# Kernel optimization log

Hardware: AMD Instinct MI355X
Metric: run time of the kernel (lower is better)

Reference implementation:

```python
import jax, jax.numpy as jnp
import numpy as np

D_MODEL = 1024
NUM_HEADS = 16
D_K = D_MODEL // NUM_HEADS


def setup_inputs() -> dict:
    key = jax.random.key(0)
    ks = jax.random.split(key, 5)
    s = 1.0 / np.sqrt(D_MODEL)
    return {
        "x": jax.random.normal(ks[0], (2, 2048, D_MODEL), dtype=jnp.float32),
        "Wq": jax.random.normal(ks[1], (D_MODEL, D_MODEL), dtype=jnp.float32) * s,
        "bq": jnp.zeros((D_MODEL,), jnp.float32),
        "Wk": jax.random.normal(ks[2], (D_MODEL, D_MODEL), dtype=jnp.float32) * s,
        "bk": jnp.zeros((D_MODEL,), jnp.float32),
        "Wv": jax.random.normal(ks[3], (D_MODEL, D_MODEL), dtype=jnp.float32) * s,
        "bv": jnp.zeros((D_MODEL,), jnp.float32),
        "Wo": jax.random.normal(ks[4], (D_MODEL, D_MODEL), dtype=jnp.float32) * s,
        "bo": jnp.zeros((D_MODEL,), jnp.float32),
    }


def _rotate_half(t):
    t1, t2 = t[..., : D_K // 2], t[..., D_K // 2 :]
    return jnp.concatenate((-t2, t1), axis=-1)


def reference(x, Wq, bq, Wk, bk, Wv, bv, Wo, bo):
    B, S, D = x.shape
    H, dk = NUM_HEADS, D_K
    # RoPE tables: inv_freq over even dims, emb = cat(freqs, freqs)
    inv_freq = 1.0 / (10000.0 ** (jnp.arange(0, dk, 2, dtype=jnp.float32) / dk))
    pos = jnp.arange(S, dtype=jnp.float32)
    freqs = pos[:, None] * inv_freq[None, :]            # [S, dk/2]
    emb = jnp.concatenate((freqs, freqs), axis=-1)      # [S, dk]
    cos = jnp.cos(emb)[None, :, None, :]                # [1, S, 1, dk]
    sin = jnp.sin(emb)[None, :, None, :]

    q = (x @ Wq + bq).reshape(B, S, H, dk)
    k = (x @ Wk + bk).reshape(B, S, H, dk)
    v = (x @ Wv + bv).reshape(B, S, H, dk)

    q = q * cos + _rotate_half(q) * sin
    k = k * cos + _rotate_half(k) * sin

    # [B,H,S,S] scores, stable softmax, then weighted sum of V
    scores = jnp.einsum("bqhd,bkhd->bhqk", q, k) / jnp.sqrt(jnp.float32(dk))
    attn = jax.nn.softmax(scores, axis=-1)
    out = jnp.einsum("bhqk,bkhd->bqhd", attn, v).reshape(B, S, D)
    return out @ Wo + bo
```

## Files before the change

### kernel.cpp

```cpp
#include <hip/hip_runtime.h>
#include <hip/hip_bf16.h>
#include <math.h>

typedef __bf16 bf16_t;
typedef bf16_t bf16x4 __attribute__((ext_vector_type(4)));
typedef bf16_t bf16x8 __attribute__((ext_vector_type(8)));
typedef float f32x4 __attribute__((ext_vector_type(4)));

#define SEQ 2048
#define BATCH 2
#define NHEAD 16
#define DK 64
#define DMODEL 1024

#define GLOAD16(gsrc, ldst)                                                        \
    __builtin_amdgcn_global_load_lds(                                              \
        (const __attribute__((address_space(1))) void*)(gsrc),                     \
        (__attribute__((address_space(3))) void*)(ldst), 16, 0, 0)

__device__ __forceinline__ float exp2_hw(float x) {
#if __has_builtin(__builtin_amdgcn_exp2f)
    return __builtin_amdgcn_exp2f(x);
#else
    float r; asm("v_exp_f32 %0, %1" : "=v"(r) : "v"(x)); return r;
#endif
}

__global__ __launch_bounds__(256)
void prep_kernel(const float* __restrict__ x, bf16_t* __restrict__ y,
                 const float* __restrict__ W0, const float* __restrict__ W1,
                 const float* __restrict__ W2, const float* __restrict__ W3,
                 bf16_t* __restrict__ Wt, float2* __restrict__ cs) {
    __shared__ float t[32][33];
    const int id = blockIdx.x, tid = threadIdx.x;
    if (id < 4096) {
        int i = (id * 256 + tid) * 4;
        float4 v = *reinterpret_cast<const float4*>(x + i);
        bf16x4 o = { (bf16_t)v.x, (bf16_t)v.y, (bf16_t)v.z, (bf16_t)v.w };
        *reinterpret_cast<bf16x4*>(y + i) = o;
    } else if (id < 8192) {
        const int id2 = id - 4096;
        const int z = id2 >> 10, rem = id2 & 1023;
        const int n0 = (rem & 31) * 32, k0 = ((rem >> 5) & 31) * 32;
        const int tx = tid & 31, ty = tid >> 5;
        const float* W = (z == 0) ? W0 : (z == 1) ? W1 : (z == 2) ? W2 : W3;
        bf16_t* out = Wt + ((size_t)z << 20);
#pragma unroll
        for (int i = 0; i < 32; i += 8)
            t[ty + i][tx] = W[(size_t)(k0 + ty + i) * DMODEL + n0 + tx];
        __syncthreads();
#pragma unroll
        for (int i = 0; i < 32; i += 8)
            out[(size_t)(n0 + ty + i) * DMODEL + k0 + tx] = (bf16_t)t[tx][ty + i];
    } else {
        int idx = (id - 8192) * 256 + tid;
        int j = idx & 31, s = idx >> 5;
        float inv = powf(10000.0f, -(float)j / 32.0f);
        float ang = (float)s * inv;
        cs[idx] = make_float2(cosf(ang), sinf(ang));
    }
}

template<int NF>
__device__ __forceinline__ void gemm_core(const bf16_t* __restrict__ A,
                                          const bf16_t* __restrict__ Bt,
                                          int m0, int n0,
                                          bf16_t* As, bf16_t* Bs,
                                          f32x4 (&acc)[4][NF]) {
    const int tid = threadIdx.x, lane = tid & 63, wid = tid >> 6;
    const int wr = wid >> 1, wc = wid & 1;
    const int lm = lane & 15, lq = lane >> 4;
    constexpr int BROWS = NF * 32;
    constexpr int NT = DMODEL / 32;

    const int r_in = lane >> 2;
    const int csw  = (((lane & 3) ^ ((lane >> 3) & 3)) << 3);
    const bf16_t* Ag = A  + (size_t)(m0 + 32 * wid + r_in) * DMODEL + csw;
    const bf16_t* Bg = Bt + (size_t)(n0 + (NF * 8) * wid + r_in) * DMODEL + csw;
    const int cswr = ((lq ^ ((lm >> 1) & 3)) << 4);

    auto stage = [&](int t, int buf) {
        const int k0 = t * 32;
        bf16_t* a = As + buf * (128 * 32) + 32 * wid * 32;
        bf16_t* b = Bs + buf * (BROWS * 32) + (NF * 8) * wid * 32;
        GLOAD16(Ag + k0,               a);
        GLOAD16(Ag + 16 * DMODEL + k0, a + 16 * 32);
        GLOAD16(Bg + k0,               b);
        if constexpr (NF == 4) GLOAD16(Bg + 16 * DMODEL + k0, b + 16 * 32);
    };

    stage(0, 0);
    stage(1, 1);
    int cb = 0;
    for (int t = 0; t < NT; ++t) {
        if (t + 2 < NT) {
            int sb = cb + 2; if (sb >= 3) sb -= 3;
            stage(t + 2, sb);
            if constexpr (NF == 4) asm volatile("s_waitcnt vmcnt(8)" ::: "memory");
            else                   asm volatile("s_waitcnt vmcnt(6)" ::: "memory");
        } else if (t + 1 < NT) {
            if constexpr (NF == 4) asm volatile("s_waitcnt vmcnt(4)" ::: "memory");
            else                   asm volatile("s_waitcnt vmcnt(3)" ::: "memory");
        } else {
            asm volatile("s_waitcnt vmcnt(0)" ::: "memory");
        }
        __builtin_amdgcn_s_barrier();

        const char* pAs = (const char*)(As + cb * (128 * 32));
        const char* pBs = (const char*)(Bs + cb * (BROWS * 32));
        bf16x8 af[4], bfr[NF];
#pragma unroll
        for (int mf = 0; mf < 4; ++mf)
            af[mf] = *reinterpret_cast<const bf16x8*>(pAs + (wr * 64 + mf * 16 + lm) * 64 + cswr);
#pragma unroll
        for (int nf = 0; nf < NF; ++nf)
            bfr[nf] = *reinterpret_cast<const bf16x8*>(pBs + (wc * (NF * 16) + nf * 16 + lm) * 64 + cswr);
#pragma unroll
        for (int mf = 0; mf < 4; ++mf)
#pragma unroll
            for (int nf = 0; nf < NF; ++nf)
                acc[mf][nf] = __builtin_amdgcn_mfma_f32_16x16x32_bf16(af[mf], bfr[nf], acc[mf][nf], 0, 0, 0);

        asm volatile("" ::: "memory");
        __builtin_amdgcn_s_barrier();
        if (++cb == 3) cb = 0;
    }
}

__global__ __launch_bounds__(256)
void gemm_qkv_kernel(const bf16_t* __restrict__ xb, const bf16_t* __restrict__ wtqk,
                     const bf16_t* __restrict__ wtv,
                     const float* __restrict__ bq, const float* __restrict__ bk,
                     const float* __restrict__ bv,
                     bf16_t* __restrict__ qb, bf16_t* __restrict__ kb,
                     bf16_t* __restrict__ vtb, const float2* __restrict__ cs) {
    __shared__ bf16_t As[3 * 128 * 32];
    __shared__ bf16_t Bs[3 * 128 * 32];
    const int tid = threadIdx.x, lane = tid & 63, wid = tid >> 6;
    const int wr = wid >> 1, wc = wid & 1;
    const int lm = lane & 15, lq = lane >> 4;
    const int orig = blockIdx.x;
    const int id = (orig & 7) * 96 + (orig >> 3);
    f32x4 acc[4][4] = {};

    if (id < 512) {
        const int m0 = (id >> 4) * 128, n0 = (id & 15) * 128;
        gemm_core<4>(xb, wtqk, m0, n0, As, Bs, acc);
        const bool is_k = (n0 >= 1024);
        const float* bs = is_k ? bk : bq;
        bf16_t* C = is_k ? kb : qb;
        const int cb = (is_k ? n0 - 1024 : n0) + wc * 64;
        const float b0 = bs[cb + lm],      b1 = bs[cb + 16 + lm];
        const float b2 = bs[cb + 32 + lm], b3 = bs[cb + 48 + lm];
#pragma unroll
        for (int mf = 0; mf < 4; ++mf)
#pragma unroll
            for (int i = 0; i < 4; ++i) {
                const int row = m0 + wr * 64 + mf * 16 + lq * 4 + i;
                const int s = row & (SEQ - 1);
                const float2 cs0 = cs[s * 32 + lm];
                const float2 cs1 = cs[s * 32 + 16 + lm];
                const float a0 = acc[mf][0][i] + b0, a1 = acc[mf][1][i] + b1;
                const float a2 = acc[mf][2][i] + b2, a3 = acc[mf][3][i] + b3;
                bf16_t* p = C + (size_t)row * DMODEL + cb;
                p[lm]      = (bf16_t)(a0 * cs0.x - a2 * cs0.y);
                p[16 + lm] = (bf16_t)(a1 * cs1.x - a3 * cs1.y);
                p[32 + lm] = (bf16_t)(a2 * cs0.x + a0 * cs0.y);
                p[48 + lm] = (bf16_t)(a3 * cs1.x + a1 * cs1.y);
            }
    } else {
        const int id2 = id - 512;
        const int m0 = (id2 & 7) * 128, n0 = (id2 >> 3) * 128;
        gemm_core<4>(wtv, xb, m0, n0, As, Bs, acc);
#pragma unroll
        for (int mf = 0; mf < 4; ++mf)
#pragma unroll
            for (int i = 0; i < 4; ++i) {
                const int row = m0 + wr * 64 + mf * 16 + lq * 4 + i;
                const float brow = bv[row];
#pragma unroll
                for (int nf = 0; nf < 4; ++nf) {
                    const int col = n0 + wc * 64 + nf * 16 + lm;
                    vtb[(size_t)row * 4096 + col] = (bf16_t)(acc[mf][nf][i] + brow);
                }
            }
    }
}

__global__ __launch_bounds__(256)
void gemm_out_kernel(const bf16_t* __restrict__ A, const bf16_t* __restrict__ Bt,
                     const float* __restrict__ bias, float* __restrict__ C) {
    __shared__ bf16_t As[3 * 128 * 32];
    __shared__ bf16_t Bs[3 * 64 * 32];
    const int tid = threadIdx.x, lane = tid & 63, wid = tid >> 6;
    const int wr = wid >> 1, wc = wid & 1;
    const int lm = lane & 15, lq = lane >> 4;
    const int orig = blockIdx.x;
    const int id = (orig & 7) * 64 + (orig >> 3);
    const int m0 = (id >> 4) * 128, n0 = (id & 15) * 64;
    f32x4 acc[4][2] = {};
    gemm_core<2>(A, Bt, m0, n0, As, Bs, acc);
#pragma unroll
    for (int nf = 0; nf < 2; ++nf) {
        const int col = n0 + wc * 32 + nf * 16 + lm;
        const float bcol = bias[col];
#pragma unroll
        for (int mf = 0; mf < 4; ++mf)
#pragma unroll
            for (int i = 0; i < 4; ++i) {
                const int row = m0 + wr * 64 + mf * 16 + lq * 4 + i;
                C[(size_t)row * DMODEL + col] = acc[mf][nf][i] + bcol;
            }
    }
}

__global__ __launch_bounds__(512)
void attn_kernel(const bf16_t* __restrict__ q, const bf16_t* __restrict__ k,
                 const bf16_t* __restrict__ vt, bf16_t* __restrict__ attnout) {
    const int tid = threadIdx.x, lane = tid & 63, wid = tid >> 6;
    const int lm = lane & 15, lq = lane >> 4;
    const int bh = blockIdx.y, b = bh >> 4, h = bh & 15;
    const int qrow0 = blockIdx.x * 128 + wid * 16;
    const float MS = 20.0f;

    __shared__ bf16_t Ks[2][64][64];
    __shared__ bf16_t Vs[2][64][64];
    __shared__ bf16_t Ps[8][16][80];

    const bf16_t* qptr = q + ((size_t)(b * SEQ + qrow0 + lm) * NHEAD + h) * DK + lq * 8;
    bf16x8 aq0 = *reinterpret_cast<const bf16x8*>(qptr);
    bf16x8 aq1 = *reinterpret_cast<const bf16x8*>(qptr + 32);
#pragma unroll
    for (int j = 0; j < 8; ++j) {
        aq0[j] = (bf16_t)((float)aq0[j] * 0.18033688f);
        aq1[j] = (bf16_t)((float)aq1[j] * 0.18033688f);
    }
    const bf16_t one = (bf16_t)1.0f;
    const bf16x8 ones = { one, one, one, one, one, one, one, one };
    const f32x4 cinit = { -MS, -MS, -MS, -MS };

    const int srow = lane >> 3;
    const int scol = (((lane & 7) ^ srow) << 3);
    const bf16_t* kg = k  + ((size_t)(b * SEQ + 8 * wid + srow) * NHEAD + h) * DK + scol;
    const bf16_t* vg = vt + ((size_t)(h * DK + 8 * wid + srow)) * 4096 + (size_t)b * SEQ + scol;

    const char* ksb = (const char*)Ks;
    const char* vsb = (const char*)Vs;
    char* pwb = (char*)&Ps[wid][0][0];
    const int c0 = (lq << 4) ^ ((lm & 7) << 4);
    const int rowb = lm * 128;
    const int psw = (lm & 7) << 4;

    f32x4 O[4] = {};
    f32x4 ol = {};

    GLOAD16(kg, &Ks[0][8 * wid][0]);
    GLOAD16(vg, &Vs[0][8 * wid][0]);

    int buf = 0;
    for (int kb = 0; kb < SEQ; kb += 64) {
        if (kb + 64 < SEQ) {
            GLOAD16(kg + (size_t)(kb + 64) * (NHEAD * DK), &Ks[buf ^ 1][8 * wid][0]);
            GLOAD16(vg + (kb + 64),                        &Vs[buf ^ 1][8 * wid][0]);
            asm volatile("s_waitcnt vmcnt(2)" ::: "memory");
        } else {
            asm volatile("s_waitcnt vmcnt(0)" ::: "memory");
        }
        __builtin_amdgcn_s_barrier();
        asm volatile("" ::: "memory");

        const char* kt  = ksb + buf * 8192;
        const char* vtl = vsb + buf * 8192;

        f32x4 st[4];
        __builtin_amdgcn_s_setprio(1);
#pragma unroll
        for (int t = 0; t < 4; ++t) {
            bf16x8 a0 = *reinterpret_cast<const bf16x8*>(kt + t * 2048 + rowb + c0);
            bf16x8 a1 = *reinterpret_cast<const bf16x8*>(kt + t * 2048 + rowb + (c0 ^ 64));
            f32x4 s = __builtin_amdgcn_mfma_f32_16x16x32_bf16(a0, aq0, cinit, 0, 0, 0);
            s = __builtin_amdgcn_mfma_f32_16x16x32_bf16(a1, aq1, s, 0, 0, 0);
            st[t] = s;
        }
        __builtin_amdgcn_s_setprio(0);

#pragma unroll
        for (int t = 0; t < 4; ++t) {
            const float e0 = exp2_hw(st[t][0]);
            const float e1 = exp2_hw(st[t][1]);
            const float e2 = exp2_hw(st[t][2]);
            const float e3 = exp2_hw(st[t][3]);
            bf16x4 c = { (bf16_t)e0, (bf16_t)e1, (bf16_t)e2, (bf16_t)e3 };
            *reinterpret_cast<bf16x4*>(pwb + lm * 160 + (((t << 5) | (lq << 3)) ^ psw)) = c;
        }

        asm volatile("s_waitcnt lgkmcnt(0)" ::: "memory");
        const bf16x8 pa0 = *reinterpret_cast<const bf16x8*>(pwb + lm * 160 + ((lq << 4) ^ psw));
        const bf16x8 pa1 = *reinterpret_cast<const bf16x8*>(pwb + lm * 160 + ((64 | (lq << 4)) ^ psw));

        __builtin_amdgcn_s_setprio(1);
#pragma unroll
        for (int nf = 0; nf < 4; ++nf) {
            bf16x8 v0 = *reinterpret_cast<const bf16x8*>(vtl + nf * 2048 + rowb + c0);
            bf16x8 v1 = *reinterpret_cast<const bf16x8*>(vtl + nf * 2048 + rowb + (c0 ^ 64));
            f32x4 o = O[nf];
            o = __builtin_amdgcn_mfma_f32_16x16x32_bf16(v0, pa0, o, 0, 0, 0);
            o = __builtin_amdgcn_mfma_f32_16x16x32_bf16(v1, pa1, o, 0, 0, 0);
            O[nf] = o;
        }
        ol = __builtin_amdgcn_mfma_f32_16x16x32_bf16(ones, pa0, ol, 0, 0, 0);
        ol = __builtin_amdgcn_mfma_f32_16x16x32_bf16(ones, pa1, ol, 0, 0, 0);
        __builtin_amdgcn_s_setprio(0);

        asm volatile("" ::: "memory");
        __builtin_amdgcn_s_barrier();
        buf ^= 1;
    }

    const float inv = 1.0f / ol[0];
    bf16_t* ob = attnout + ((size_t)(b * SEQ + qrow0 + lm) * NHEAD + h) * DK;
#pragma unroll
    for (int nf = 0; nf < 4; ++nf) {
        bf16x4 c = { (bf16_t)(O[nf][0] * inv), (bf16_t)(O[nf][1] * inv),
                     (bf16_t)(O[nf][2] * inv), (bf16_t)(O[nf][3] * inv) };
        *reinterpret_cast<bf16x4*>(ob + nf * 16 + lq * 4) = c;
    }
}

extern "C" void kernel_launch(void* const* d_in, const int* in_sizes, int n_in,
                              void* d_out, int out_size, void* d_ws, size_t ws_size,
                              hipStream_t stream) {
    const float* x  = (const float*)d_in[0];
    const float* Wq = (const float*)d_in[1];
    const float* bq = (const float*)d_in[2];
    const float* Wk = (const float*)d_in[3];
    const float* bk = (const float*)d_in[4];
    const float* Wv = (const float*)d_in[5];
    const float* bv = (const float*)d_in[6];
    const float* Wo = (const float*)d_in[7];
    const float* bo = (const float*)d_in[8];
    float* out = (float*)d_out;

    char* ws = (char*)d_ws;
    bf16_t* xb  = (bf16_t*)(ws);
    bf16_t* wtq = (bf16_t*)(ws + ((size_t)8  << 20));
    bf16_t* wtv = wtq + (2 << 20);
    bf16_t* wto = wtq + (3 << 20);
    bf16_t* qb  = (bf16_t*)(ws + ((size_t)16 << 20));
    bf16_t* kb  = (bf16_t*)(ws + ((size_t)24 << 20));
    bf16_t* vtb = (bf16_t*)(ws + ((size_t)32 << 20));
    float2* csT = (float2*)(ws + ((size_t)40 << 20));
    bf16_t* aob = xb;

    prep_kernel<<<8448, 256, 0, stream>>>(x, xb, Wq, Wk, Wv, Wo, wtq, csT);
    gemm_qkv_kernel<<<768, 256, 0, stream>>>(xb, wtq, wtv, bq, bk, bv, qb, kb, vtb, csT);
    attn_kernel<<<dim3(16, 32), 512, 0, stream>>>(qb, kb, vtb, aob);
    gemm_out_kernel<<<512, 256, 0, stream>>>(aob, wto, bo, out);
}
```

Before: 124.7 us.

## Process two query tiles per wave and keep P in registers via permuted K rows

Each attention block now runs 4 waves of 32 query rows instead of 8 waves of 16, so every K/V fragment read from LDS feeds two MFMA chains. The K tile is loaded with a permuted row mapping so the score MFMA output layout lines up directly with the B-operand layout of the PV MFMA. This drops the per-wave shared-memory round trip for the softmax probabilities and its lgkmcnt wait. The cost is more registers per wave and half as many waves per block for hiding latency.

```diff
diff --git a/kernel.cpp b/kernel.cpp
--- a/kernel.cpp
+++ b/kernel.cpp
@@ -214,55 +214,63 @@
     }
 }
 
-__global__ __launch_bounds__(512)
+__global__ __launch_bounds__(256)
 void attn_kernel(const bf16_t* __restrict__ q, const bf16_t* __restrict__ k,
                  const bf16_t* __restrict__ vt, bf16_t* __restrict__ attnout) {
     const int tid = threadIdx.x, lane = tid & 63, wid = tid >> 6;
     const int lm = lane & 15, lq = lane >> 4;
     const int bh = blockIdx.y, b = bh >> 4, h = bh & 15;
-    const int qrow0 = blockIdx.x * 128 + wid * 16;
+    const int qrow0 = blockIdx.x * 128 + wid * 32;
     const float MS = 20.0f;
 
     __shared__ bf16_t Ks[2][64][64];
     __shared__ bf16_t Vs[2][64][64];
-    __shared__ bf16_t Ps[8][16][80];
-
-    const bf16_t* qptr = q + ((size_t)(b * SEQ + qrow0 + lm) * NHEAD + h) * DK + lq * 8;
-    bf16x8 aq0 = *reinterpret_cast<const bf16x8*>(qptr);
-    bf16x8 aq1 = *reinterpret_cast<const bf16x8*>(qptr + 32);
+
+    const bf16_t* qA = q + ((size_t)(b * SEQ + qrow0 + lm) * NHEAD + h) * DK + lq * 8;
+    const bf16_t* qB = qA + (size_t)16 * NHEAD * DK;
+    bf16x8 aqA0 = *reinterpret_cast<const bf16x8*>(qA);
+    bf16x8 aqA1 = *reinterpret_cast<const bf16x8*>(qA + 32);
+    bf16x8 aqB0 = *reinterpret_cast<const bf16x8*>(qB);
+    bf16x8 aqB1 = *reinterpret_cast<const bf16x8*>(qB + 32);
 #pragma unroll
     for (int j = 0; j < 8; ++j) {
-        aq0[j] = (bf16_t)((float)aq0[j] * 0.18033688f);
-        aq1[j] = (bf16_t)((float)aq1[j] * 0.18033688f);
+        aqA0[j] = (bf16_t)((float)aqA0[j] * 0.18033688f);
+        aqA1[j] = (bf16_t)((float)aqA1[j] * 0.18033688f);
+        aqB0[j] = (bf16_t)((float)aqB0[j] * 0.18033688f);
+        aqB1[j] = (bf16_t)((float)aqB1[j] * 0.18033688f);
     }
     const bf16_t one = (bf16_t)1.0f;
     const bf16x8 ones = { one, one, one, one, one, one, one, one };
     const f32x4 cinit = { -MS, -MS, -MS, -MS };
 
-    const int srow = lane >> 3;
-    const int scol = (((lane & 7) ^ srow) << 3);
-    const bf16_t* kg = k  + ((size_t)(b * SEQ + 8 * wid + srow) * NHEAD + h) * DK + scol;
-    const bf16_t* vg = vt + ((size_t)(h * DK + 8 * wid + srow)) * 4096 + (size_t)b * SEQ + scol;
-
+    const int r0   = 8 * wid + (lane >> 3);
+    const int scol = (((lane & 7) ^ (lane >> 3)) << 3);
+    const int sig  = ((r0 >> 2) & 3) * 8 + ((r0 >> 4) & 1) * 4 + (r0 & 3);
+    const bf16_t* kg = k  + ((size_t)(b * SEQ + sig) * NHEAD + h) * DK + scol;
+    const bf16_t* vg = vt + ((size_t)(h * DK + r0)) * 4096 + (size_t)b * SEQ + scol;
+    const size_t kstep = (size_t)NHEAD * DK;
     const char* ksb = (const char*)Ks;
     const char* vsb = (const char*)Vs;
-    char* pwb = (char*)&Ps[wid][0][0];
     const int c0 = (lq << 4) ^ ((lm & 7) << 4);
     const int rowb = lm * 128;
-    const int psw = (lm & 7) << 4;
-
-    f32x4 O[4] = {};
-    f32x4 ol = {};
-
-    GLOAD16(kg, &Ks[0][8 * wid][0]);
-    GLOAD16(vg, &Vs[0][8 * wid][0]);
+
+    f32x4 OA[4] = {}, OB[4] = {};
+    f32x4 olA = {}, olB = {};
+
+    auto stage = [&](int buf, int kb) {
+        GLOAD16(kg + (size_t)kb * kstep,        &Ks[buf][8 * wid][0]);
+        GLOAD16(kg + (size_t)(kb + 32) * kstep, &Ks[buf][32 + 8 * wid][0]);
+        GLOAD16(vg + kb,                        &Vs[buf][8 * wid][0]);
+        GLOAD16(vg + (size_t)32 * 4096 + kb,    &Vs[buf][32 + 8 * wid][0]);
+    };
+
+    stage(0, 0);
 
     int buf = 0;
     for (int kb = 0; kb < SEQ; kb += 64) {
         if (kb + 64 < SEQ) {
-            GLOAD16(kg + (size_t)(kb + 64) * (NHEAD * DK), &Ks[buf ^ 1][8 * wid][0]);
-            GLOAD16(vg + (kb + 64),                        &Vs[buf ^ 1][8 * wid][0]);
-            asm volatile("s_waitcnt vmcnt(2)" ::: "memory");
+            stage(buf ^ 1, kb + 64);
+            asm volatile("s_waitcnt vmcnt(4)" ::: "memory");
         } else {
             asm volatile("s_waitcnt vmcnt(0)" ::: "memory");
         }
@@ -272,44 +280,47 @@
         const char* kt  = ksb + buf * 8192;
         const char* vtl = vsb + buf * 8192;
 
-        f32x4 st[4];
+        f32x4 stA[4], stB[4];
         __builtin_amdgcn_s_setprio(1);
 #pragma unroll
         for (int t = 0; t < 4; ++t) {
             bf16x8 a0 = *reinterpret_cast<const bf16x8*>(kt + t * 2048 + rowb + c0);
             bf16x8 a1 = *reinterpret_cast<const bf16x8*>(kt + t * 2048 + rowb + (c0 ^ 64));
-            f32x4 s = __builtin_amdgcn_mfma_f32_16x16x32_bf16(a0, aq0, cinit, 0, 0, 0);
-            s = __builtin_amdgcn_mfma_f32_16x16x32_bf16(a1, aq1, s, 0, 0, 0);
-            st[t] = s;
+            f32x4 sA = __builtin_amdgcn_mfma_f32_16x16x32_bf16(a0, aqA0, cinit, 0, 0, 0);
+            sA = __builtin_amdgcn_mfma_f32_16x16x32_bf16(a1, aqA1, sA, 0, 0, 0);
+            f32x4 sB = __builtin_amdgcn_mfma_f32_16x16x32_bf16(a0, aqB0, cinit, 0, 0, 0);
+            sB = __builtin_amdgcn_mfma_f32_16x16x32_bf16(a1, aqB1, sB, 0, 0, 0);
+            stA[t] = sA; stB[t] = sB;
         }
         __builtin_amdgcn_s_setprio(0);
 
-#pragma unroll
-        for (int t = 0; t < 4; ++t) {
-            const float e0 = exp2_hw(st[t][0]);
-            const float e1 = exp2_hw(st[t][1]);
-            const float e2 = exp2_hw(st[t][2]);
-            const float e3 = exp2_hw(st[t][3]);
-            bf16x4 c = { (bf16_t)e0, (bf16_t)e1, (bf16_t)e2, (bf16_t)e3 };
-            *reinterpret_cast<bf16x4*>(pwb + lm * 160 + (((t << 5) | (lq << 3)) ^ psw)) = c;
-        }
-
-        asm volatile("s_waitcnt lgkmcnt(0)" ::: "memory");
-        const bf16x8 pa0 = *reinterpret_cast<const bf16x8*>(pwb + lm * 160 + ((lq << 4) ^ psw));
-        const bf16x8 pa1 = *reinterpret_cast<const bf16x8*>(pwb + lm * 160 + ((64 | (lq << 4)) ^ psw));
+        bf16x8 paA0, paA1, paB0, paB1;
+#pragma unroll
+        for (int t = 0; t < 2; ++t)
+#pragma unroll
+            for (int i = 0; i < 4; ++i) {
+                paA0[4 * t + i] = (bf16_t)exp2_hw(stA[t][i]);
+                paA1[4 * t + i] = (bf16_t)exp2_hw(stA[t + 2][i]);
+                paB0[4 * t + i] = (bf16_t)exp2_hw(stB[t][i]);
+                paB1[4 * t + i] = (bf16_t)exp2_hw(stB[t + 2][i]);
+            }
 
         __builtin_amdgcn_s_setprio(1);
 #pragma unroll
         for (int nf = 0; nf < 4; ++nf) {
             bf16x8 v0 = *reinterpret_cast<const bf16x8*>(vtl + nf * 2048 + rowb + c0);
             bf16x8 v1 = *reinterpret_cast<const bf16x8*>(vtl + nf * 2048 + rowb + (c0 ^ 64));
-            f32x4 o = O[nf];
-            o = __builtin_amdgcn_mfma_f32_16x16x32_bf16(v0, pa0, o, 0, 0, 0);
-            o = __builtin_amdgcn_mfma_f32_16x16x32_bf16(v1, pa1, o, 0, 0, 0);
-            O[nf] = o;
+            f32x4 oA = OA[nf], oB = OB[nf];
+            oA = __builtin_amdgcn_mfma_f32_16x16x32_bf16(v0, paA0, oA, 0, 0, 0);
+            oA = __builtin_amdgcn_mfma_f32_16x16x32_bf16(v1, paA1, oA, 0, 0, 0);
+            oB = __builtin_amdgcn_mfma_f32_16x16x32_bf16(v0, paB0, oB, 0, 0, 0);
+            oB = __builtin_amdgcn_mfma_f32_16x16x32_bf16(v1, paB1, oB, 0, 0, 0);
+            OA[nf] = oA; OB[nf] = oB;
         }
-        ol = __builtin_amdgcn_mfma_f32_16x16x32_bf16(ones, pa0, ol, 0, 0, 0);
-        ol = __builtin_amdgcn_mfma_f32_16x16x32_bf16(ones, pa1, ol, 0, 0, 0);
+        olA = __builtin_amdgcn_mfma_f32_16x16x32_bf16(ones, paA0, olA, 0, 0, 0);
+        olA = __builtin_amdgcn_mfma_f32_16x16x32_bf16(ones, paA1, olA, 0, 0, 0);
+        olB = __builtin_amdgcn_mfma_f32_16x16x32_bf16(ones, paB0, olB, 0, 0, 0);
+        olB = __builtin_amdgcn_mfma_f32_16x16x32_bf16(ones, paB1, olB, 0, 0, 0);
         __builtin_amdgcn_s_setprio(0);
 
         asm volatile("" ::: "memory");
@@ -317,13 +328,18 @@
         buf ^= 1;
     }
 
-    const float inv = 1.0f / ol[0];
-    bf16_t* ob = attnout + ((size_t)(b * SEQ + qrow0 + lm) * NHEAD + h) * DK;
+    const float invA = 1.0f / olA[0];
+    const float invB = 1.0f / olB[0];
+    bf16_t* obA = attnout + ((size_t)(b * SEQ + qrow0 + lm) * NHEAD + h) * DK;
+    bf16_t* obB = obA + (size_t)16 * NHEAD * DK;
 #pragma unroll
     for (int nf = 0; nf < 4; ++nf) {
-        bf16x4 c = { (bf16_t)(O[nf][0] * inv), (bf16_t)(O[nf][1] * inv),
-                     (bf16_t)(O[nf][2] * inv), (bf16_t)(O[nf][3] * inv) };
-        *reinterpret_cast<bf16x4*>(ob + nf * 16 + lq * 4) = c;
+        bf16x4 cA = { (bf16_t)(OA[nf][0] * invA), (bf16_t)(OA[nf][1] * invA),
+                      (bf16_t)(OA[nf][2] * invA), (bf16_t)(OA[nf][3] * invA) };
+        bf16x4 cB = { (bf16_t)(OB[nf][0] * invB), (bf16_t)(OB[nf][1] * invB),
+                      (bf16_t)(OB[nf][2] * invB), (bf16_t)(OB[nf][3] * invB) };
+        *reinterpret_cast<bf16x4*>(obA + nf * 16 + lq * 4) = cA;
+        *reinterpret_cast<bf16x4*>(obB + nf * 16 + lq * 4) = cB;
     }
 }
 
@@ -354,6 +370,6 @@
 
     prep_kernel<<<8448, 256, 0, stream>>>(x, xb, Wq, Wk, Wv, Wo, wtq, csT);
     gemm_qkv_kernel<<<768, 256, 0, stream>>>(xb, wtq, wtv, bq, bk, bv, qb, kb, vtb, csT);
-    attn_kernel<<<dim3(16, 32), 512, 0, stream>>>(qb, kb, vtb, aob);
+    attn_kernel<<<dim3(16, 32), 256, 0, stream>>>(qb, kb, vtb, aob);
     gemm_out_kernel<<<512, 256, 0, stream>>>(aob, wto, bo, out);
 }
```

Result: no change. 124.8 us (+0.1%).

## Restructure attention to 64 query rows per wave with register-resident P

Applied to the files above, without the earlier changes.

The attention kernel now gives each wave 4 query subtiles of 16 rows, so each K/V fragment read from LDS is reused four times. The kernel moves to 256-thread blocks with XCD-aware block mapping and a 4-deep K/V LDS ring holding two tiles in flight. A permuted K-row load order lets the exp'd scores feed the PV MFMA directly from registers, removing the P round-trip through LDS. Row sums are accumulated in scalar registers and reduced with shuffles instead of a ones-MFMA. The output GEMM switches to 128x128 tiles with half as many blocks; the larger tiles raise register pressure and cut the block count to 256, which may hurt occupancy.

```diff
diff --git a/kernel.cpp b/kernel.cpp
--- a/kernel.cpp
+++ b/kernel.cpp
@@ -191,18 +191,18 @@
 void gemm_out_kernel(const bf16_t* __restrict__ A, const bf16_t* __restrict__ Bt,
                      const float* __restrict__ bias, float* __restrict__ C) {
     __shared__ bf16_t As[3 * 128 * 32];
-    __shared__ bf16_t Bs[3 * 64 * 32];
+    __shared__ bf16_t Bs[3 * 128 * 32];
     const int tid = threadIdx.x, lane = tid & 63, wid = tid >> 6;
     const int wr = wid >> 1, wc = wid & 1;
     const int lm = lane & 15, lq = lane >> 4;
     const int orig = blockIdx.x;
-    const int id = (orig & 7) * 64 + (orig >> 3);
-    const int m0 = (id >> 4) * 128, n0 = (id & 15) * 64;
-    f32x4 acc[4][2] = {};
-    gemm_core<2>(A, Bt, m0, n0, As, Bs, acc);
-#pragma unroll
-    for (int nf = 0; nf < 2; ++nf) {
-        const int col = n0 + wc * 32 + nf * 16 + lm;
+    const int id = (orig & 7) * 32 + (orig >> 3);
+    const int m0 = (id >> 3) * 128, n0 = (id & 7) * 128;
+    f32x4 acc[4][4] = {};
+    gemm_core<4>(A, Bt, m0, n0, As, Bs, acc);
+#pragma unroll
+    for (int nf = 0; nf < 4; ++nf) {
+        const int col = n0 + wc * 64 + nf * 16 + lm;
         const float bcol = bias[col];
 #pragma unroll
         for (int mf = 0; mf < 4; ++mf)
@@ -214,116 +214,141 @@
     }
 }
 
-__global__ __launch_bounds__(512)
+__global__ __launch_bounds__(256)
 void attn_kernel(const bf16_t* __restrict__ q, const bf16_t* __restrict__ k,
                  const bf16_t* __restrict__ vt, bf16_t* __restrict__ attnout) {
     const int tid = threadIdx.x, lane = tid & 63, wid = tid >> 6;
     const int lm = lane & 15, lq = lane >> 4;
-    const int bh = blockIdx.y, b = bh >> 4, h = bh & 15;
-    const int qrow0 = blockIdx.x * 128 + wid * 16;
+    const int bid = blockIdx.x;
+    const int xcd = bid & 7, idx = bid >> 3;
+    const int bh = xcd * 4 + (idx & 3), qblk = idx >> 2;
+    const int b = bh >> 4, h = bh & 15;
+    const int qrow0 = qblk * 256 + wid * 64;
     const float MS = 20.0f;
-
-    __shared__ bf16_t Ks[2][64][64];
-    __shared__ bf16_t Vs[2][64][64];
-    __shared__ bf16_t Ps[8][16][80];
-
-    const bf16_t* qptr = q + ((size_t)(b * SEQ + qrow0 + lm) * NHEAD + h) * DK + lq * 8;
-    bf16x8 aq0 = *reinterpret_cast<const bf16x8*>(qptr);
-    bf16x8 aq1 = *reinterpret_cast<const bf16x8*>(qptr + 32);
-#pragma unroll
-    for (int j = 0; j < 8; ++j) {
-        aq0[j] = (bf16_t)((float)aq0[j] * 0.18033688f);
-        aq1[j] = (bf16_t)((float)aq1[j] * 0.18033688f);
-    }
-    const bf16_t one = (bf16_t)1.0f;
-    const bf16x8 ones = { one, one, one, one, one, one, one, one };
+    constexpr int NT = SEQ / 64;
+
+    __shared__ bf16_t Ks[4][64][64];
+    __shared__ bf16_t Vs[4][64][64];
+
+    const bf16_t* qp = q + ((size_t)(b * SEQ + qrow0 + lm) * NHEAD + h) * DK + lq * 8;
+    bf16x8 aq[4][2];
+#pragma unroll
+    for (int s = 0; s < 4; ++s) {
+        aq[s][0] = *reinterpret_cast<const bf16x8*>(qp + (size_t)(16 * s) * NHEAD * DK);
+        aq[s][1] = *reinterpret_cast<const bf16x8*>(qp + (size_t)(16 * s) * NHEAD * DK + 32);
+#pragma unroll
+        for (int j = 0; j < 8; ++j) {
+            aq[s][0][j] = (bf16_t)((float)aq[s][0][j] * 0.18033688f);
+            aq[s][1][j] = (bf16_t)((float)aq[s][1][j] * 0.18033688f);
+        }
+    }
     const f32x4 cinit = { -MS, -MS, -MS, -MS };
 
-    const int srow = lane >> 3;
-    const int scol = (((lane & 7) ^ srow) << 3);
-    const bf16_t* kg = k  + ((size_t)(b * SEQ + 8 * wid + srow) * NHEAD + h) * DK + scol;
-    const bf16_t* vg = vt + ((size_t)(h * DK + 8 * wid + srow)) * 4096 + (size_t)b * SEQ + scol;
-
+    const int rr = lane >> 3;
+    const int scol = (((lane & 7) ^ rr) << 3);
+    const int r0 = 16 * wid + rr, r1 = r0 + 8;
+    const int sg0 = (r0 & 32) | (((r0 >> 2) & 3) * 8 + ((r0 >> 4) & 1) * 4 + (r0 & 3));
+    const int sg1 = (r1 & 32) | (((r1 >> 2) & 3) * 8 + ((r1 >> 4) & 1) * 4 + (r1 & 3));
+    const size_t kstep = (size_t)NHEAD * DK;
+    const bf16_t* kg0 = k + ((size_t)(b * SEQ + sg0) * NHEAD + h) * DK + scol;
+    const bf16_t* kg1 = k + ((size_t)(b * SEQ + sg1) * NHEAD + h) * DK + scol;
+    const bf16_t* vg0 = vt + ((size_t)(h * DK + r0)) * 4096 + (size_t)b * SEQ + scol;
+    const bf16_t* vg1 = vt + ((size_t)(h * DK + r1)) * 4096 + (size_t)b * SEQ + scol;
     const char* ksb = (const char*)Ks;
     const char* vsb = (const char*)Vs;
-    char* pwb = (char*)&Ps[wid][0][0];
     const int c0 = (lq << 4) ^ ((lm & 7) << 4);
     const int rowb = lm * 128;
-    const int psw = (lm & 7) << 4;
-
-    f32x4 O[4] = {};
-    f32x4 ol = {};
-
-    GLOAD16(kg, &Ks[0][8 * wid][0]);
-    GLOAD16(vg, &Vs[0][8 * wid][0]);
-
-    int buf = 0;
-    for (int kb = 0; kb < SEQ; kb += 64) {
-        if (kb + 64 < SEQ) {
-            GLOAD16(kg + (size_t)(kb + 64) * (NHEAD * DK), &Ks[buf ^ 1][8 * wid][0]);
-            GLOAD16(vg + (kb + 64),                        &Vs[buf ^ 1][8 * wid][0]);
-            asm volatile("s_waitcnt vmcnt(2)" ::: "memory");
+
+    f32x4 O[4][4] = {};
+    float rs[4] = {};
+
+    auto stage = [&](int buf, int kb) {
+        GLOAD16(kg0 + (size_t)kb * kstep, &Ks[buf][16 * wid][0]);
+        GLOAD16(kg1 + (size_t)kb * kstep, &Ks[buf][16 * wid + 8][0]);
+        GLOAD16(vg0 + kb,                 &Vs[buf][16 * wid][0]);
+        GLOAD16(vg1 + kb,                 &Vs[buf][16 * wid + 8][0]);
+    };
+
+    stage(0, 0);
+    stage(1, 64);
+
+    for (int t = 0; t < NT; ++t) {
+        if (t + 2 < NT) {
+            stage((t + 2) & 3, (t + 2) * 64);
+            asm volatile("s_waitcnt vmcnt(8)" ::: "memory");
+        } else if (t + 1 < NT) {
+            asm volatile("s_waitcnt vmcnt(4)" ::: "memory");
         } else {
             asm volatile("s_waitcnt vmcnt(0)" ::: "memory");
         }
         __builtin_amdgcn_s_barrier();
         asm volatile("" ::: "memory");
 
-        const char* kt  = ksb + buf * 8192;
-        const char* vtl = vsb + buf * 8192;
-
-        f32x4 st[4];
-        __builtin_amdgcn_s_setprio(1);
-#pragma unroll
-        for (int t = 0; t < 4; ++t) {
-            bf16x8 a0 = *reinterpret_cast<const bf16x8*>(kt + t * 2048 + rowb + c0);
-            bf16x8 a1 = *reinterpret_cast<const bf16x8*>(kt + t * 2048 + rowb + (c0 ^ 64));
-            f32x4 s = __builtin_amdgcn_mfma_f32_16x16x32_bf16(a0, aq0, cinit, 0, 0, 0);
-            s = __builtin_amdgcn_mfma_f32_16x16x32_bf16(a1, aq1, s, 0, 0, 0);
-            st[t] = s;
-        }
-        __builtin_amdgcn_s_setprio(0);
-
-#pragma unroll
-        for (int t = 0; t < 4; ++t) {
-            const float e0 = exp2_hw(st[t][0]);
-            const float e1 = exp2_hw(st[t][1]);
-            const float e2 = exp2_hw(st[t][2]);
-            const float e3 = exp2_hw(st[t][3]);
-            bf16x4 c = { (bf16_t)e0, (bf16_t)e1, (bf16_t)e2, (bf16_t)e3 };
-            *reinterpret_cast<bf16x4*>(pwb + lm * 160 + (((t << 5) | (lq << 3)) ^ psw)) = c;
-        }
-
-        asm volatile("s_waitcnt lgkmcnt(0)" ::: "memory");
-        const bf16x8 pa0 = *reinterpret_cast<const bf16x8*>(pwb + lm * 160 + ((lq << 4) ^ psw));
-        const bf16x8 pa1 = *reinterpret_cast<const bf16x8*>(pwb + lm * 160 + ((64 | (lq << 4)) ^ psw));
-
-        __builtin_amdgcn_s_setprio(1);
-#pragma unroll
-        for (int nf = 0; nf < 4; ++nf) {
-            bf16x8 v0 = *reinterpret_cast<const bf16x8*>(vtl + nf * 2048 + rowb + c0);
-            bf16x8 v1 = *reinterpret_cast<const bf16x8*>(vtl + nf * 2048 + rowb + (c0 ^ 64));
-            f32x4 o = O[nf];
-            o = __builtin_amdgcn_mfma_f32_16x16x32_bf16(v0, pa0, o, 0, 0, 0);
-            o = __builtin_amdgcn_mfma_f32_16x16x32_bf16(v1, pa1, o, 0, 0, 0);
-            O[nf] = o;
-        }
-        ol = __builtin_amdgcn_mfma_f32_16x16x32_bf16(ones, pa0, ol, 0, 0, 0);
-        ol = __builtin_amdgcn_mfma_f32_16x16x32_bf16(ones, pa1, ol, 0, 0, 0);
-        __builtin_amdgcn_s_setprio(0);
+        const char* kt  = ksb + (t & 3) * 8192;
+        const char* vtl = vsb + (t & 3) * 8192;
+
+        bf16x8 a0[4], a1[4], v0[4], v1[4];
+#pragma unroll
+        for (int u = 0; u < 4; ++u) {
+            a0[u] = *reinterpret_cast<const bf16x8*>(kt + u * 2048 + rowb + c0);
+            a1[u] = *reinterpret_cast<const bf16x8*>(kt + u * 2048 + rowb + (c0 ^ 64));
+            v0[u] = *reinterpret_cast<const bf16x8*>(vtl + u * 2048 + rowb + c0);
+            v1[u] = *reinterpret_cast<const bf16x8*>(vtl + u * 2048 + rowb + (c0 ^ 64));
+        }
+
+#pragma unroll
+        for (int s = 0; s < 4; ++s) {
+            f32x4 st[4];
+            __builtin_amdgcn_s_setprio(1);
+#pragma unroll
+            for (int u = 0; u < 4; ++u) {
+                f32x4 x = __builtin_amdgcn_mfma_f32_16x16x32_bf16(a0[u], aq[s][0], cinit, 0, 0, 0);
+                st[u] = __builtin_amdgcn_mfma_f32_16x16x32_bf16(a1[u], aq[s][1], x, 0, 0, 0);
+            }
+            __builtin_amdgcn_s_setprio(0);
+
+            bf16x8 pa0, pa1;
+            float acc = 0.f;
+#pragma unroll
+            for (int u = 0; u < 2; ++u)
+#pragma unroll
+                for (int i = 0; i < 4; ++i) {
+                    const float e0 = exp2_hw(st[u][i]);
+                    const float e1 = exp2_hw(st[u + 2][i]);
+                    acc += e0 + e1;
+                    pa0[4 * u + i] = (bf16_t)e0;
+                    pa1[4 * u + i] = (bf16_t)e1;
+                }
+            rs[s] += acc;
+
+            __builtin_amdgcn_s_setprio(1);
+#pragma unroll
+            for (int nf = 0; nf < 4; ++nf) {
+                f32x4 o = O[s][nf];
+                o = __builtin_amdgcn_mfma_f32_16x16x32_bf16(v0[nf], pa0, o, 0, 0, 0);
+                o = __builtin_amdgcn_mfma_f32_16x16x32_bf16(v1[nf], pa1, o, 0, 0, 0);
+                O[s][nf] = o;
+            }
+            __builtin_amdgcn_s_setprio(0);
+        }
 
         asm volatile("" ::: "memory");
         __builtin_amdgcn_s_barrier();
-        buf ^= 1;
-    }
-
-    const float inv = 1.0f / ol[0];
-    bf16_t* ob = attnout + ((size_t)(b * SEQ + qrow0 + lm) * NHEAD + h) * DK;
-#pragma unroll
-    for (int nf = 0; nf < 4; ++nf) {
-        bf16x4 c = { (bf16_t)(O[nf][0] * inv), (bf16_t)(O[nf][1] * inv),
-                     (bf16_t)(O[nf][2] * inv), (bf16_t)(O[nf][3] * inv) };
-        *reinterpret_cast<bf16x4*>(ob + nf * 16 + lq * 4) = c;
+    }
+
+#pragma unroll
+    for (int s = 0; s < 4; ++s) {
+        float rt = rs[s];
+        rt += __shfl_xor(rt, 16, 64);
+        rt += __shfl_xor(rt, 32, 64);
+        const float inv = 1.0f / rt;
+        bf16_t* ob = attnout + ((size_t)(b * SEQ + qrow0 + s * 16 + lm) * NHEAD + h) * DK;
+#pragma unroll
+        for (int nf = 0; nf < 4; ++nf) {
+            bf16x4 c = { (bf16_t)(O[s][nf][0] * inv), (bf16_t)(O[s][nf][1] * inv),
+                         (bf16_t)(O[s][nf][2] * inv), (bf16_t)(O[s][nf][3] * inv) };
+            *reinterpret_cast<bf16x4*>(ob + nf * 16 + lq * 4) = c;
+        }
     }
 }
 
@@ -354,6 +379,6 @@
 
     prep_kernel<<<8448, 256, 0, stream>>>(x, xb, Wq, Wk, Wv, Wo, wtq, csT);
     gemm_qkv_kernel<<<768, 256, 0, stream>>>(xb, wtq, wtv, bq, bk, bv, qb, kb, vtb, csT);
-    attn_kernel<<<dim3(16, 32), 512, 0, stream>>>(qb, kb, vtb, aob);
-    gemm_out_kernel<<<512, 256, 0, stream>>>(aob, wto, bo, out);
-}
+    attn_kernel<<<256, 256, 0, stream>>>(qb, kb, vtb, aob);
+    gemm_out_kernel<<<256, 256, 0, stream>>>(aob, wto, bo, out);
+}
```

After: 142.2 us. 14.1% more time.
